# Optimization experiments

Hardware: AMD Instinct MI355X
Metric: run time of the kernel (lower is better)

Reference implementation:

```python
import jax, jax.numpy as jnp
import numpy as np

B, N, M, K = 4, 16384, 16384, 16   # batch, points, centers, neighbors
C, O, G = 64, 64, 8                # in_planes, out_planes, group


def setup_inputs() -> dict:
    key = jax.random.key(0)
    ks = jax.random.split(key, 16)
    r = lambda i, sh, s=1.0: jax.random.normal(ks[i], sh, jnp.float32) * s
    return dict(
        center_pos=r(0, (B, M, 3)),
        center_fea=r(1, (B, C, M)),
        pos=r(2, (B, N, 3)),
        fea=r(3, (B, C, N)),
        idx=jax.random.randint(ks[4], (B, M, K), 0, N, jnp.int32),
        # linear q/k/v
        Wq=r(5, (C, O), 0.05), bq=jnp.zeros((O,), jnp.float32),
        Wk=r(6, (C, O), 0.05), bk=jnp.zeros((O,), jnp.float32),
        Wv=r(7, (C, O), 0.05), bv=jnp.zeros((O,), jnp.float32),
        # center_pos_encode: conv1x1(3->O, no bias) + folded BN (scale,shift) + relu + conv1x1(O->O)
        cpe_w1=r(8, (3, O), 0.05), cpe_s=jnp.ones((O,), jnp.float32), cpe_b=jnp.zeros((O,), jnp.float32),
        cpe_w2=r(9, (O, O), 0.05), cpe_b2=jnp.zeros((O,), jnp.float32),
        # pos_encode (Conv2d 1x1 == per-point linear)
        pe_w1=r(10, (3, O), 0.05), pe_s=jnp.ones((O,), jnp.float32), pe_b=jnp.zeros((O,), jnp.float32),
        pe_w2=r(11, (O, O), 0.05), pe_b2=jnp.zeros((O,), jnp.float32),
        # weight_encode (O -> G)
        we_w1=r(12, (O, G), 0.05), we_s=jnp.ones((G,), jnp.float32), we_b=jnp.zeros((G,), jnp.float32),
        we_w2=r(13, (G, G), 0.05), we_b2=jnp.zeros((G,), jnp.float32),
    )


def _mlp2(x, w1, s, b, w2, b2):
    # conv1x1(no bias) -> inference BatchNorm folded to (scale, shift) -> ReLU -> conv1x1(+bias)
    h = jax.nn.relu(x @ w1 * s + b)
    return h @ w2 + b2


def reference(center_pos, center_fea, pos, fea, idx,
              Wq, bq, Wk, bk, Wv, bv,
              cpe_w1, cpe_s, cpe_b, cpe_w2, cpe_b2,
              pe_w1, pe_s, pe_b, pe_w2, pe_b2,
              we_w1, we_s, we_b, we_w2, we_b2):
    x_q = center_fea.transpose(0, 2, 1) @ Wq + bq        # [B,M,O]
    ft = fea.transpose(0, 2, 1)                          # [B,N,C]
    x_k = ft @ Wk + bk                                   # [B,N,O]
    x_v = ft @ Wv + bv                                   # [B,N,O]

    gather = jax.vmap(lambda a, i: a[i])                 # per-batch irregular gather
    nk = gather(x_k, idx)                                # [B,M,K,O]
    nv = gather(x_v, idx)                                # [B,M,K,O]
    npos = gather(pos, idx) - center_pos[:, :, None, :]  # [B,M,K,3] relative coords

    cpr = _mlp2(center_pos, cpe_w1, cpe_s, cpe_b, cpe_w2, cpe_b2)  # [B,M,O]
    pr = _mlp2(npos, pe_w1, pe_s, pe_b, pe_w2, pe_b2)              # [B,M,K,O]

    r_qk = nk - x_q[:, :, None, :] + cpr[:, :, None, :]  # [B,M,K,O]
    v = nv + pr                                          # [B,M,K,O]

    w = _mlp2(r_qk, we_w1, we_s, we_b, we_w2, we_b2)     # [B,M,K,G]
    w = jax.nn.softmax(w, axis=2)                        # softmax over neighbors

    v = v.reshape(B, M, K, G, O // G)
    out = jnp.einsum('bmkgi,bmkg->bmgi', v, w).reshape(B, M, O)
    return out.transpose(0, 2, 1)                        # [B,O,M]
```

## Files before the change

kernel.cpp:

```cpp
#include <hip/hip_runtime.h>
#include <hip/hip_bf16.h>

typedef unsigned short u16;
typedef __attribute__((ext_vector_type(8))) __bf16 bf8v;
typedef __attribute__((ext_vector_type(8))) _Float16 f16x8;
typedef __attribute__((ext_vector_type(2))) _Float16 h2v;
typedef __attribute__((ext_vector_type(4))) float f32x4;
typedef __attribute__((ext_vector_type(4))) unsigned uint4v;

#define B_ 4
#define N_ 16384
#define M_ 16384
#define K_ 16
#define C_ 64
#define O_ 64
#define G_ 8

__device__ __forceinline__ float bf2f(u16 x){
  union { unsigned u; float f; } v; v.u = ((unsigned)x) << 16; return v.f;
}
__device__ __forceinline__ u16 f2bf(float f){
  union { float f; unsigned u; } v; v.f = f;
  unsigned u = v.u;
  return (u16)((u + 0x7FFFu + ((u >> 16) & 1u)) >> 16);
}
__device__ __forceinline__ u16 f2h(float f){
  union { _Float16 h; u16 u; } v; v.h = (_Float16)f; return v.u;
}
__device__ __forceinline__ h2v mkh2(float a, float b){
  h2v r = {(_Float16)a, (_Float16)b}; return r;
}

__global__ __launch_bounds__(256) void pre_kernel(
    const float* __restrict__ center_pos, const float* __restrict__ center_fea,
    const float* __restrict__ pos, const float* __restrict__ fea,
    const float* __restrict__ Wq, const float* __restrict__ bq,
    const float* __restrict__ Wk, const float* __restrict__ bk,
    const float* __restrict__ Wv, const float* __restrict__ bv,
    const float* __restrict__ cpe_w1, const float* __restrict__ cpe_s, const float* __restrict__ cpe_b,
    const float* __restrict__ cpe_w2, const float* __restrict__ cpe_b2,
    const float* __restrict__ we_w1,
    u16* __restrict__ xk, u16* __restrict__ xv, float* __restrict__ qw,
    float* __restrict__ pos4, float* __restrict__ cp4)
{
  __shared__ u16 sWT[128*72];
  __shared__ u16 sA[64*72];
  __shared__ u16 sOut[64*136];
  __shared__ float sMisc[256];
  __shared__ float sCi[8];
  int tid = threadIdx.x;
  int l = tid & 63, w = tid >> 6, c = l & 15, q = l >> 4;
  int blk = blockIdx.x;

  if (blk < 256){
    int P0 = blk * 256; int b = P0 >> 14; int n00 = P0 & (N_-1);
    const float* fb = fea + (long)b*C_*N_;
    for (int e = tid; e < 8192; e += 256){
      int k = e >> 7, col = e & 127;
      float v = (col < 64) ? Wk[k*64 + col] : Wv[k*64 + (col-64)];
      sWT[col*72 + k] = f2bf(v);
    }
    if (tid < 128) sMisc[tid] = (tid < 64) ? bk[tid] : bv[tid-64];
    {
      long pg = (long)P0 + tid;
      f32x4 r = {pos[pg*3], pos[pg*3+1], pos[pg*3+2], 0.f};
      ((f32x4*)pos4)[pg] = r;
    }

    #pragma unroll 1
    for (int s = 0; s < 4; s++){
      int n0 = n00 + s*64;
      #pragma unroll
      for (int pp = 0; pp < 4; pp++){
        int k = pp*16 + (tid >> 4);
        int nf = (tid & 15)*4;
        f32x4 v = *(const f32x4*)&fb[(long)k*N_ + n0 + nf];
        sA[(nf+0)*72+k] = f2bf(v[0]); sA[(nf+1)*72+k] = f2bf(v[1]);
        sA[(nf+2)*72+k] = f2bf(v[2]); sA[(nf+3)*72+k] = f2bf(v[3]);
      }
      __syncthreads();

      bf8v af0 = *(const bf8v*)&sA[(w*16+c)*72 + q*8];
      bf8v af1 = *(const bf8v*)&sA[(w*16+c)*72 + 32 + q*8];
      f32x4 acc[8];
      #pragma unroll
      for (int t = 0; t < 8; t++){
        float bb = sMisc[16*t + c];
        f32x4 a_ = {bb, bb, bb, bb};
        bf8v b0 = *(const bf8v*)&sWT[(16*t + c)*72 + q*8];
        bf8v b1 = *(const bf8v*)&sWT[(16*t + c)*72 + 32 + q*8];
        a_ = __builtin_amdgcn_mfma_f32_16x16x32_bf16(af0, b0, a_, 0,0,0);
        a_ = __builtin_amdgcn_mfma_f32_16x16x32_bf16(af1, b1, a_, 0,0,0);
        acc[t] = a_;
      }
      #pragma unroll
      for (int t = 0; t < 8; t++)
        #pragma unroll
        for (int r = 0; r < 4; r++)
          sOut[(w*16 + q*4 + r)*136 + 16*t + c] = f2bf(acc[t][r]);
      __syncthreads();

      #pragma unroll
      for (int rep = 0; rep < 4; rep++){
        int chunk = rep*256 + tid;
        int pt = chunk >> 4, c8i = chunk & 15;
        uint4v val = *(const uint4v*)&sOut[pt*136 + c8i*8];
        int col8 = c8i*8;
        long row = (long)P0 + s*64 + pt;
        if (col8 < 64) *(uint4v*)(xk + row*64 + col8)      = val;
        else           *(uint4v*)(xv + row*64 + (col8-64)) = val;
      }
      __syncthreads();
    }
  } else {
    int P0 = (blk - 256) * 256; int b = P0 >> 14; int m00 = P0 & (M_-1);
    const float* cfb = center_fea + (long)b*C_*M_;
    float* sWe = (float*)sOut;
    float* sQ  = (float*)sOut;
    for (int e = tid; e < 512; e += 256) sWe[e] = we_w1[e];
    if (tid < 64){
      float sc = cpe_s[tid];
      sMisc[tid]     = cpe_w1[tid]*sc;
      sMisc[64+tid]  = cpe_w1[64+tid]*sc;
      sMisc[128+tid] = cpe_w1[128+tid]*sc;
      sMisc[192+tid] = cpe_b[tid];
    }
    {
      long pg = (long)P0 + tid;
      f32x4 r = {center_pos[pg*3], center_pos[pg*3+1], center_pos[pg*3+2], 0.f};
      ((f32x4*)cp4)[pg] = r;
    }
    __syncthreads();
    {
      int k = tid >> 1, g0 = (tid & 1)*4;
      const float* brow = (k < 64) ? (cpe_w2 + k*64) : (Wq + (k-64)*64);
      float sgn = (k < 64) ? 1.f : -1.f;
      float aw[4] = {0.f,0.f,0.f,0.f};
      for (int o = 0; o < 64; o++){
        float bo = brow[o]*sgn;
        #pragma unroll
        for (int gg=0; gg<4; gg++) aw[gg] += bo * sWe[o*8 + g0+gg];
      }
      #pragma unroll
      for (int gg=0; gg<4; gg++) sWT[(g0+gg)*136 + k] = f2bf(aw[gg]);
    }
    for (int e = tid; e < 2176; e += 256){
      int r = e / 136, cc = e % 136;
      if (r >= 8 || cc >= 128) sWT[e] = 0;
    }
    if (tid < 8){
      float s = 0.f;
      for (int o = 0; o < 64; o++) s += (cpe_b2[o] - bq[o]) * sWe[o*8 + tid];
      sCi[tid] = s;
    }
    __syncthreads();

    #pragma unroll 1
    for (int s = 0; s < 4; s++){
      int m0 = m00 + s*64;
      #pragma unroll
      for (int pp = 0; pp < 4; pp++){
        int k = pp*16 + (tid >> 4);
        int nf = (tid & 15)*4;
        f32x4 v = *(const f32x4*)&cfb[(long)k*M_ + m0 + nf];
        sA[(nf+0)*72+k] = f2bf(v[0]); sA[(nf+1)*72+k] = f2bf(v[1]);
        sA[(nf+2)*72+k] = f2bf(v[2]); sA[(nf+3)*72+k] = f2bf(v[3]);
      }
      long c3 = (long)(P0 + s*64 + w*16 + c)*3;
      float cp0 = center_pos[c3], cp1 = center_pos[c3+1], cp2 = center_pos[c3+2];
      __syncthreads();

      bf8v ah[2];
      #pragma unroll
      for (int ks = 0; ks < 2; ks++){
        union { bf8v v; u16 sv[8]; } ua;
        #pragma unroll
        for (int j = 0; j < 8; j++){
          int h = ks*32 + q*8 + j;
          float hv = cp0*sMisc[h] + cp1*sMisc[64+h] + cp2*sMisc[128+h] + sMisc[192+h];
          ua.sv[j] = f2bf(fmaxf(hv, 0.f));
        }
        ah[ks] = ua.v;
      }
      bf8v acf0 = *(const bf8v*)&sA[(w*16+c)*72 + q*8];
      bf8v acf1 = *(const bf8v*)&sA[(w*16+c)*72 + 32 + q*8];

      float ci = (c < 8) ? sCi[c] : 0.f;
      f32x4 aq = {ci, ci, ci, ci};
      {
        bf8v b0 = *(const bf8v*)&sWT[c*136 + q*8];
        bf8v b1 = *(const bf8v*)&sWT[c*136 + 32 + q*8];
        bf8v b2 = *(const bf8v*)&sWT[c*136 + 64 + q*8];
        bf8v b3 = *(const bf8v*)&sWT[c*136 + 96 + q*8];
        aq = __builtin_amdgcn_mfma_f32_16x16x32_bf16(ah[0], b0, aq, 0,0,0);
        aq = __builtin_amdgcn_mfma_f32_16x16x32_bf16(ah[1], b1, aq, 0,0,0);
        aq = __builtin_amdgcn_mfma_f32_16x16x32_bf16(acf0,  b2, aq, 0,0,0);
        aq = __builtin_amdgcn_mfma_f32_16x16x32_bf16(acf1,  b3, aq, 0,0,0);
      }
      __syncthreads();
      if (c < 8){
        #pragma unroll
        for (int r = 0; r < 4; r++) sQ[(w*16 + q*4 + r)*8 + c] = aq[r];
      }
      __syncthreads();
      for (int e = tid; e < 512; e += 256)
        qw[(long)(P0 + s*64)*8 + e] = sQ[e];
      __syncthreads();
    }
  }
}

__global__ __launch_bounds__(256) void attn_kernel(
    const float* __restrict__ cp4, const float* __restrict__ pos4,
    const int* __restrict__ idx,
    const float* __restrict__ pe_w1, const float* __restrict__ pe_s, const float* __restrict__ pe_b,
    const float* __restrict__ pe_w2, const float* __restrict__ pe_b2,
    const float* __restrict__ we_w1, const float* __restrict__ we_s, const float* __restrict__ we_b,
    const float* __restrict__ we_w2, const float* __restrict__ we_b2,
    const u16* __restrict__ xk, const u16* __restrict__ xv, const float* __restrict__ qw,
    float* __restrict__ out)
{
  int tid = threadIdx.x;
  __shared__ float s_w1f[192], s_pb[64], s_pb2[64], s_ww2[64];
  __shared__ float s_ws8[8], s_wb8[8], s_wb28[8];
  __shared__ f32x4 s_dyn4[1312];
  __shared__ float s_tile[32*66];

  char* dynb = (char*)s_dyn4;

  if (tid < 64){
    float sc = pe_s[tid];
    s_w1f[tid]     = pe_w1[tid]*sc;
    s_w1f[64+tid]  = pe_w1[64+tid]*sc;
    s_w1f[128+tid] = pe_w1[128+tid]*sc;
    s_pb[tid]  = pe_b[tid];
    s_pb2[tid] = pe_b2[tid];
    s_ww2[tid] = we_w2[tid];
  }
  if (tid >= 64 && tid < 72){
    int g = tid-64;
    s_ws8[g]=we_s[g]; s_wb8[g]=we_b[g]; s_wb28[g]=we_b2[g];
  }
  u16* stg = (u16*)dynb;
  #pragma unroll
  for (int pp = 0; pp < 4; pp++){
    int row = pp*16 + (tid >> 4);
    int colf = (tid & 15)*4;
    f32x4 v = *(const f32x4*)&pe_w2[row*64 + colf];
    stg[(colf+0)*72+row] = f2h(v[0]); stg[(colf+1)*72+row] = f2h(v[1]);
    stg[(colf+2)*72+row] = f2h(v[2]); stg[(colf+3)*72+row] = f2h(v[3]);
  }
  u16* stg2 = (u16*)(dynb + 9216);
  for (int e = tid; e < 512; e += 256){
    int k = e >> 3, cc = e & 7;
    stg2[cc*72 + k] = f2bf(we_w1[e]);
  }
  for (int e = tid; e < 576; e += 256) stg2[576 + e] = 0;
  __syncthreads();

  int w = tid >> 6, l = tid & 63, c = l & 15, q = l >> 4, c8 = c & 7, qb = l & 48;

  f16x8 pw2f[4][2];
  bf8v ww1f[2];
  f16x8 w2B, hz8;
  #pragma unroll
  for (int t = 0; t < 4; t++){
    pw2f[t][0] = *(const f16x8*)&stg[(t*16+c)*72 + q*8];
    pw2f[t][1] = *(const f16x8*)&stg[(t*16+c)*72 + 32 + q*8];
  }
  ww1f[0] = *(const bf8v*)&stg2[c*72 + q*8];
  ww1f[1] = *(const bf8v*)&stg2[c*72 + 32 + q*8];
  {
    union { f16x8 v; u16 s[8]; } uu;
    #pragma unroll
    for (int j = 0; j < 8; j++)
      uu.s[j] = (q == 0 && c < 8) ? f2h(s_ww2[j*8 + c]) : (u16)0;
    w2B = uu.v;
    #pragma unroll
    for (int j = 0; j < 8; j++) uu.s[j] = 0;
    hz8 = uu.v;
  }
  h2v cw0[2][4], cw1[2][4], cw2[2][4], cb[2][4];
  #pragma unroll
  for (int ks = 0; ks < 2; ks++)
    #pragma unroll
    for (int jj = 0; jj < 4; jj++){
      int o = ks*32 + q*8 + jj*2;
      cw0[ks][jj] = mkh2(s_w1f[o],     s_w1f[o+1]);
      cw1[ks][jj] = mkh2(s_w1f[64+o],  s_w1f[65+o]);
      cw2[ks][jj] = mkh2(s_w1f[128+o], s_w1f[129+o]);
      cb [ks][jj] = mkh2(s_pb[o],      s_pb[o+1]);
    }
  float ws_c = s_ws8[c8], wb_c = s_wb8[c8], wb2_c = s_wb28[c8];
  float pb2l = s_pb2[l];
  h2v hz2 = {(_Float16)0.f, (_Float16)0.f};
  __syncthreads();

  float* sv  = (float*)(dynb + w*5248);
  float* swt = (float*)(dynb + w*5248 + 4352);
  u16*  sh   = (u16*) (dynb + w*5248 + 4992);

  int pbase = blockIdx.x * 32;
  int b = pbase >> 14;
  const u16* xkb = xk + (long)b * N_ * 64;
  const u16* xvb = xv + (long)b * N_ * 64;
  const f32x4* pos4b = ((const f32x4*)pos4) + (long)b * N_;
  int ch = c >> 3;
  int gl = l >> 3;

  int pb0 = pbase + w*8;
  const int*   idxl = idx + (long)pb0*16 + c;
  const float* qwl  = qw  + (long)pb0*8 + c8;
  const f32x4* cp4l = ((const f32x4*)cp4) + pb0;

  int iv = idxl[0];
  float qpv = qwl[0];
  f32x4 cpv = cp4l[0];
  f32x4 ppv = pos4b[iv];
  const u16* kr0 = xkb + (size_t)iv*64;
  bf8v ka0 = *(const bf8v*)(kr0 + q*8);
  bf8v ka1 = *(const bf8v*)(kr0 + 32 + q*8);
  const u16* vr0 = xvb + (size_t)iv*64;
  uint4v va0 = *(const uint4v*)(vr0 + q*8);
  uint4v va1 = *(const uint4v*)(vr0 + 32 + q*8);

  #pragma unroll 1
  for (int i = 0; i < 8; i++){
    int ni = (i < 7) ? i+1 : i;
    int iv_n = idxl[ni*16];
    float qpv_n = qwl[ni*8];
    f32x4 cpn = cp4l[ni];
    f32x4 ppn = pos4b[iv_n];
    const u16* krn = xkb + (size_t)iv_n*64;
    bf8v kan0 = *(const bf8v*)(krn + q*8);
    bf8v kan1 = *(const bf8v*)(krn + 32 + q*8);
    const u16* vrn = xvb + (size_t)iv_n*64;
    uint4v van0 = *(const uint4v*)(vrn + q*8);
    uint4v van1 = *(const uint4v*)(vrn + 32 + q*8);

    {
      f32x4 f0, f1, f2, f3;
      #pragma unroll
      for (int jj = 0; jj < 2; jj++){
        unsigned u0 = va0[jj*2], u1 = va0[jj*2+1];
        f0[jj*2]   = bf2f((u16)u0); f0[jj*2+1] = bf2f((u16)(u0>>16));
        f1[jj*2]   = bf2f((u16)u1); f1[jj*2+1] = bf2f((u16)(u1>>16));
      }
      unsigned a0 = va0[0], a1 = va0[1], a2 = va0[2], a3 = va0[3];
      f32x4 lo0 = {bf2f((u16)a0), bf2f((u16)(a0>>16)), bf2f((u16)a1), bf2f((u16)(a1>>16))};
      f32x4 hi0 = {bf2f((u16)a2), bf2f((u16)(a2>>16)), bf2f((u16)a3), bf2f((u16)(a3>>16))};
      unsigned b0 = va1[0], b1 = va1[1], b2 = va1[2], b3 = va1[3];
      f32x4 lo1 = {bf2f((u16)b0), bf2f((u16)(b0>>16)), bf2f((u16)b1), bf2f((u16)(b1>>16))};
      f32x4 hi1 = {bf2f((u16)b2), bf2f((u16)(b2>>16)), bf2f((u16)b3), bf2f((u16)(b3>>16))};
      f32x4* d0 = (f32x4*)&sv[c*68 + q*8];
      d0[0] = lo0; d0[1] = hi0;
      f32x4* d1 = (f32x4*)&sv[c*68 + 32 + q*8];
      d1[0] = lo1; d1[1] = hi1;
    }

    float np0 = ppv[0] - cpv[0], np1 = ppv[1] - cpv[1], np2 = ppv[2] - cpv[2];
    h2v np0h = {(_Float16)np0, (_Float16)np0};
    h2v np1h = {(_Float16)np1, (_Float16)np1};
    h2v np2h = {(_Float16)np2, (_Float16)np2};
    f16x8 h1f[2];
    #pragma unroll
    for (int ks = 0; ks < 2; ks++){
      union { f16x8 v; h2v p[4]; } hu;
      #pragma unroll
      for (int jj = 0; jj < 4; jj++){
        h2v a = cb[ks][jj];
        a = np0h*cw0[ks][jj] + a;
        a = np1h*cw1[ks][jj] + a;
        a = np2h*cw2[ks][jj] + a;
        hu.p[jj] = __builtin_elementwise_max(a, hz2);
      }
      h1f[ks] = hu.v;
    }

    f32x4 h2a = {qpv, qpv, qpv, qpv};
    h2a = __builtin_amdgcn_mfma_f32_16x16x32_bf16(ka0, ww1f[0], h2a, 0,0,0);
    h2a = __builtin_amdgcn_mfma_f32_16x16x32_bf16(ka1, ww1f[1], h2a, 0,0,0);

    if (c < 8){
      #pragma unroll
      for (int r = 0; r < 4; r++)
        sh[(q*4+r)*8 + c] = f2h(fmaxf(h2a[r]*ws_c + wb_c, 0.f));
    }
    f16x8 hrow = *(const f16x8*)&sh[c*8];
    f16x8 ahf = (q == 0) ? hrow : hz8;

    f32x4 wlv = {wb2_c, wb2_c, wb2_c, wb2_c};
    wlv = __builtin_amdgcn_mfma_f32_16x16x32_f16(ahf, w2B, wlv, 0,0,0);

    float e0 = exp2f(wlv[0]*1.44269504f);
    float e1 = exp2f(wlv[1]*1.44269504f);
    float e2 = exp2f(wlv[2]*1.44269504f);
    float e3 = exp2f(wlv[3]*1.44269504f);
    float sm = e0+e1+e2+e3;
    sm += __shfl_xor(sm, 16, 64);
    sm += __shfl_xor(sm, 32, 64);
    float rn = 1.0f / sm;
    if (c < 8){
      f32x4 ev = {e0*rn, e1*rn, e2*rn, e3*rn};
      *(f32x4*)&swt[c*20 + q*4] = ev;
    }

    float ov[4];
    #pragma unroll
    for (int t = 0; t < 4; t++){
      f32x4 z = {0.f,0.f,0.f,0.f};
      z = __builtin_amdgcn_mfma_f32_16x16x32_f16(h1f[0], pw2f[t][0], z, 0,0,0);
      z = __builtin_amdgcn_mfma_f32_16x16x32_f16(h1f[1], pw2f[t][1], z, 0,0,0);
      f32x4 wv = *(const f32x4*)&swt[(t*2+ch)*20 + q*4];
      ov[t] = z[0]*wv[0] + z[1]*wv[1] + z[2]*wv[2] + z[3]*wv[3];
    }
    #pragma unroll
    for (int t = 0; t < 4; t++){
      ov[t] += __shfl_xor(ov[t], 16, 64);
      ov[t] += __shfl_xor(ov[t], 32, 64);
    }
    float ovsel = ov[0];
    ovsel = (q==1) ? ov[1] : ovsel;
    ovsel = (q==2) ? ov[2] : ovsel;
    ovsel = (q==3) ? ov[3] : ovsel;

    float vacc = 0.f;
    {
      const f32x4* wr4 = (const f32x4*)&swt[gl*20];
      const float* svl = &sv[l];
      #pragma unroll
      for (int k4 = 0; k4 < 4; k4++){
        f32x4 wv = wr4[k4];
        vacc += svl[(4*k4+0)*68]*wv[0];
        vacc += svl[(4*k4+1)*68]*wv[1];
        vacc += svl[(4*k4+2)*68]*wv[2];
        vacc += svl[(4*k4+3)*68]*wv[3];
      }
    }

    s_tile[(w*8+i)*66 + l] = ovsel + vacc + pb2l;

    iv = iv_n; qpv = qpv_n; cpv = cpn; ppv = ppn;
    ka0 = kan0; ka1 = kan1; va0 = van0; va1 = van1;
  }
  __syncthreads();

  int o0 = tid >> 5, pt = tid & 31;
  int m0 = pbase & (M_-1);
  long outb = ((long)b*64) * M_ + m0 + pt;
  #pragma unroll
  for (int ii = 0; ii < 8; ii++){
    int o = o0*8 + ii;
    out[outb + (long)o*M_] = s_tile[pt*66 + o];
  }
}

extern "C" void kernel_launch(void* const* d_in, const int* in_sizes, int n_in,
                              void* d_out, int out_size, void* d_ws, size_t ws_size,
                              hipStream_t stream) {
  const float* center_pos = (const float*)d_in[0];
  const float* center_fea = (const float*)d_in[1];
  const float* pos        = (const float*)d_in[2];
  const float* fea        = (const float*)d_in[3];
  const int*   idx        = (const int*)d_in[4];
  const float* Wq = (const float*)d_in[5];   const float* bq = (const float*)d_in[6];
  const float* Wk = (const float*)d_in[7];   const float* bk = (const float*)d_in[8];
  const float* Wv = (const float*)d_in[9];   const float* bv = (const float*)d_in[10];
  const float* cpe_w1 = (const float*)d_in[11]; const float* cpe_s = (const float*)d_in[12];
  const float* cpe_b  = (const float*)d_in[13]; const float* cpe_w2 = (const float*)d_in[14];
  const float* cpe_b2 = (const float*)d_in[15];
  const float* pe_w1 = (const float*)d_in[16]; const float* pe_s = (const float*)d_in[17];
  const float* pe_b  = (const float*)d_in[18]; const float* pe_w2 = (const float*)d_in[19];
  const float* pe_b2 = (const float*)d_in[20];
  const float* we_w1 = (const float*)d_in[21]; const float* we_s = (const float*)d_in[22];
  const float* we_b  = (const float*)d_in[23]; const float* we_w2 = (const float*)d_in[24];
  const float* we_b2 = (const float*)d_in[25];

  const size_t SZ = (size_t)B_*N_*64;
  u16* xk = (u16*)d_ws;
  u16* xv = xk + SZ;
  float* qwp = (float*)(xv + SZ);
  float* pos4p = qwp + (size_t)B_*M_*8;
  float* cp4p  = pos4p + (size_t)B_*N_*4;
  float* outp = (float*)d_out;

  hipLaunchKernelGGL(pre_kernel, dim3(512), dim3(256), 0, stream,
      center_pos, center_fea, pos, fea, Wq, bq, Wk, bk, Wv, bv,
      cpe_w1, cpe_s, cpe_b, cpe_w2, cpe_b2, we_w1,
      xk, xv, qwp, pos4p, cp4p);
  hipLaunchKernelGGL(attn_kernel, dim3(2048), dim3(256), 0, stream,
      cp4p, pos4p, idx, pe_w1, pe_s, pe_b, pe_w2, pe_b2,
      we_w1, we_s, we_b, we_w2, we_b2, xk, xv, qwp, outp);
}
```

Measured before the change: 208.1 us.

## Move pos-encode weights to LDS, batch index loads, unroll prefetch loop

```diff
diff --git a/kernel.cpp b/kernel.cpp
--- a/kernel.cpp
+++ b/kernel.cpp
@@ -210,7 +210,7 @@
   }
 }
 
-__global__ __launch_bounds__(256) void attn_kernel(
+__global__ __launch_bounds__(256, 4) void attn_kernel(
     const float* __restrict__ cp4, const float* __restrict__ pos4,
     const int* __restrict__ idx,
     const float* __restrict__ pe_w1, const float* __restrict__ pe_s, const float* __restrict__ pe_b,
@@ -223,6 +223,7 @@
   int tid = threadIdx.x;
   __shared__ float s_w1f[192], s_pb[64], s_pb2[64], s_ww2[64];
   __shared__ float s_ws8[8], s_wb8[8], s_wb28[8];
+  __shared__ u16 s_pw2[64*72];
   __shared__ f32x4 s_dyn4[1312];
   __shared__ float s_tile[32*66];
 
@@ -241,16 +242,15 @@
     int g = tid-64;
     s_ws8[g]=we_s[g]; s_wb8[g]=we_b[g]; s_wb28[g]=we_b2[g];
   }
-  u16* stg = (u16*)dynb;
   #pragma unroll
   for (int pp = 0; pp < 4; pp++){
     int row = pp*16 + (tid >> 4);
     int colf = (tid & 15)*4;
     f32x4 v = *(const f32x4*)&pe_w2[row*64 + colf];
-    stg[(colf+0)*72+row] = f2h(v[0]); stg[(colf+1)*72+row] = f2h(v[1]);
-    stg[(colf+2)*72+row] = f2h(v[2]); stg[(colf+3)*72+row] = f2h(v[3]);
-  }
-  u16* stg2 = (u16*)(dynb + 9216);
+    s_pw2[(colf+0)*72+row] = f2h(v[0]); s_pw2[(colf+1)*72+row] = f2h(v[1]);
+    s_pw2[(colf+2)*72+row] = f2h(v[2]); s_pw2[(colf+3)*72+row] = f2h(v[3]);
+  }
+  u16* stg2 = (u16*)dynb;
   for (int e = tid; e < 512; e += 256){
     int k = e >> 3, cc = e & 7;
     stg2[cc*72 + k] = f2bf(we_w1[e]);
@@ -258,16 +258,10 @@
   for (int e = tid; e < 576; e += 256) stg2[576 + e] = 0;
   __syncthreads();
 
-  int w = tid >> 6, l = tid & 63, c = l & 15, q = l >> 4, c8 = c & 7, qb = l & 48;
-
-  f16x8 pw2f[4][2];
+  int w = tid >> 6, l = tid & 63, c = l & 15, q = l >> 4, c8 = c & 7;
+
   bf8v ww1f[2];
   f16x8 w2B, hz8;
-  #pragma unroll
-  for (int t = 0; t < 4; t++){
-    pw2f[t][0] = *(const f16x8*)&stg[(t*16+c)*72 + q*8];
-    pw2f[t][1] = *(const f16x8*)&stg[(t*16+c)*72 + 32 + q*8];
-  }
   ww1f[0] = *(const bf8v*)&stg2[c*72 + q*8];
   ww1f[1] = *(const bf8v*)&stg2[c*72 + 32 + q*8];
   {
@@ -309,43 +303,50 @@
   int gl = l >> 3;
 
   int pb0 = pbase + w*8;
-  const int*   idxl = idx + (long)pb0*16 + c;
-  const float* qwl  = qw  + (long)pb0*8 + c8;
+  const int*   idxp = idx + (long)pb0*16 + c;
+  const float* qwp  = qw  + (long)pb0*8 + c8;
   const f32x4* cp4l = ((const f32x4*)cp4) + pb0;
 
-  int iv = idxl[0];
-  float qpv = qwl[0];
-  f32x4 cpv = cp4l[0];
-  f32x4 ppv = pos4b[iv];
-  const u16* kr0 = xkb + (size_t)iv*64;
-  bf8v ka0 = *(const bf8v*)(kr0 + q*8);
-  bf8v ka1 = *(const bf8v*)(kr0 + 32 + q*8);
-  const u16* vr0 = xvb + (size_t)iv*64;
-  uint4v va0 = *(const uint4v*)(vr0 + q*8);
-  uint4v va1 = *(const uint4v*)(vr0 + 32 + q*8);
-
-  #pragma unroll 1
+  int idxs[8]; float qws[8];
+  #pragma unroll
+  for (int i = 0; i < 8; i++){ idxs[i] = idxp[i*16]; qws[i] = qwp[i*8]; }
+
+  f32x4 cpB[2], ppB[2];
+  bf8v kA0[2], kA1[2];
+  uint4v vA0[2], vA1[2];
+  {
+    int iv = idxs[0];
+    cpB[0] = cp4l[0];
+    ppB[0] = pos4b[iv];
+    const u16* kr = xkb + (size_t)iv*64;
+    kA0[0] = *(const bf8v*)(kr + q*8);
+    kA1[0] = *(const bf8v*)(kr + 32 + q*8);
+    const u16* vr = xvb + (size_t)iv*64;
+    vA0[0] = *(const uint4v*)(vr + q*8);
+    vA1[0] = *(const uint4v*)(vr + 32 + q*8);
+  }
+
+  #pragma unroll
   for (int i = 0; i < 8; i++){
-    int ni = (i < 7) ? i+1 : i;
-    int iv_n = idxl[ni*16];
-    float qpv_n = qwl[ni*8];
-    f32x4 cpn = cp4l[ni];
-    f32x4 ppn = pos4b[iv_n];
-    const u16* krn = xkb + (size_t)iv_n*64;
-    bf8v kan0 = *(const bf8v*)(krn + q*8);
-    bf8v kan1 = *(const bf8v*)(krn + 32 + q*8);
-    const u16* vrn = xvb + (size_t)iv_n*64;
-    uint4v van0 = *(const uint4v*)(vrn + q*8);
-    uint4v van1 = *(const uint4v*)(vrn + 32 + q*8);
+    if (i < 7){
+      int bn = (i+1)&1;
+      int ivn = idxs[i+1];
+      cpB[bn] = cp4l[i+1];
+      ppB[bn] = pos4b[ivn];
+      const u16* krn = xkb + (size_t)ivn*64;
+      kA0[bn] = *(const bf8v*)(krn + q*8);
+      kA1[bn] = *(const bf8v*)(krn + 32 + q*8);
+      const u16* vrn = xvb + (size_t)ivn*64;
+      vA0[bn] = *(const uint4v*)(vrn + q*8);
+      vA1[bn] = *(const uint4v*)(vrn + 32 + q*8);
+    }
+    int bi = i&1;
+    f32x4 cpv = cpB[bi], ppv = ppB[bi];
+    bf8v ka0 = kA0[bi], ka1 = kA1[bi];
+    uint4v va0 = vA0[bi], va1 = vA1[bi];
+    float qpv = qws[i];
 
     {
-      f32x4 f0, f1, f2, f3;
-      #pragma unroll
-      for (int jj = 0; jj < 2; jj++){
-        unsigned u0 = va0[jj*2], u1 = va0[jj*2+1];
-        f0[jj*2]   = bf2f((u16)u0); f0[jj*2+1] = bf2f((u16)(u0>>16));
-        f1[jj*2]   = bf2f((u16)u1); f1[jj*2+1] = bf2f((u16)(u1>>16));
-      }
       unsigned a0 = va0[0], a1 = va0[1], a2 = va0[2], a3 = va0[3];
       f32x4 lo0 = {bf2f((u16)a0), bf2f((u16)(a0>>16)), bf2f((u16)a1), bf2f((u16)(a1>>16))};
       f32x4 hi0 = {bf2f((u16)a2), bf2f((u16)(a2>>16)), bf2f((u16)a3), bf2f((u16)(a3>>16))};
@@ -408,9 +409,11 @@
     float ov[4];
     #pragma unroll
     for (int t = 0; t < 4; t++){
+      f16x8 pw0 = *(const f16x8*)&s_pw2[(t*16+c)*72 + q*8];
+      f16x8 pw1 = *(const f16x8*)&s_pw2[(t*16+c)*72 + 32 + q*8];
       f32x4 z = {0.f,0.f,0.f,0.f};
-      z = __builtin_amdgcn_mfma_f32_16x16x32_f16(h1f[0], pw2f[t][0], z, 0,0,0);
-      z = __builtin_amdgcn_mfma_f32_16x16x32_f16(h1f[1], pw2f[t][1], z, 0,0,0);
+      z = __builtin_amdgcn_mfma_f32_16x16x32_f16(h1f[0], pw0, z, 0,0,0);
+      z = __builtin_amdgcn_mfma_f32_16x16x32_f16(h1f[1], pw1, z, 0,0,0);
       f32x4 wv = *(const f32x4*)&swt[(t*2+ch)*20 + q*4];
       ov[t] = z[0]*wv[0] + z[1]*wv[1] + z[2]*wv[2] + z[3]*wv[3];
     }
@@ -439,9 +442,6 @@
     }
 
     s_tile[(w*8+i)*66 + l] = ovsel + vacc + pb2l;
-
-    iv = iv_n; qpv = qpv_n; cpv = cpn; ppv = ppn;
-    ka0 = kan0; ka1 = kan1; va0 = van0; va1 = van1;
   }
   __syncthreads();
 
```

New measurement: 242.8 us. 1.17x slower.
